# Optimization experiments

Measured on AMD Instinct MI355X. Metric: run time of the kernel, lower is better.

Reference implementation:

```python
import jax, jax.numpy as jnp
import numpy as np

K = 10  # module init kwarg k; Kmin selects k+1 then drops the self-distance column


def setup_inputs() -> dict:
    key = jax.random.key(0)
    N, D = 16384, 512
    obs = jax.random.normal(key, (N, D), dtype=jnp.float32)
    return {"obs": obs}


def reference(obs):
    # sa_ent=False -> x = y = obs
    x = obs
    # (same math as ((x_i - y_j)**2).sum(), expressed as a dense GEMM)
    sq = jnp.sum(x * x, axis=-1)  # [N]
    d2 = sq[:, None] + sq[None, :] - 2.0 * (x @ x.T)  # [N, N]
    # k+1 smallest per row (self-distance 0 included), ascending order
    neg_vals, _ = jax.lax.top_k(-d2, K + 1)  # [N, K+1]
    smallest = -neg_vals
    # drop self column, clamp tiny negatives from the expansion, sqrt
    r = jnp.sqrt(jnp.maximum(smallest[:, 1:], 0.0))  # [N, K]
    # style == 'log_mean'
    return jnp.log1p(jnp.mean(r, axis=-1))  # [N]
```

## Files before the change

### kernel.cpp

```cpp
#include <hip/hip_runtime.h>
#include <math.h>

#define NPTS 16384
#define DIM  512
#define KSEL 11
#define NSPLIT 8
#define CPS   (NPTS / NSPLIT)
#define BMM   256
#define BMT   128
#define BN    64
#define MITERS (CPS / BN)
#define TITERS 16
#define TCH   4096
#define STRIPB 8192
#define CAP   24
#define QS    22.0f

typedef __attribute__((ext_vector_type(4))) int i32x4;

__device__ __forceinline__ void gload_lds16(const void* g, void* l) {
    __builtin_amdgcn_global_load_lds(
        (const __attribute__((address_space(1))) void*)g,
        (__attribute__((address_space(3))) void*)l, 16, 0, 0);
}

__device__ __forceinline__ void pinreg(i32x4& v) { asm volatile("" : "+v"(v)); }
__device__ __forceinline__ void pini(int& v)     { asm volatile("" : "+v"(v)); }

__device__ __forceinline__ int topk_scan_i(const int* v, int n, int* a) {
    #pragma unroll
    for (int p = 0; p < KSEL; ++p) a[p] = v[p];
    int mx = a[0];
    #pragma unroll
    for (int p = 1; p < KSEL; ++p) mx = max(mx, a[p]);
    for (int i = KSEL; i < n; ++i) {
        const int x = v[i];
        if (x < mx) {
            bool done = false;
            #pragma unroll
            for (int p = 0; p < KSEL; ++p) {
                const bool rep = (!done) && (a[p] == mx);
                a[p] = rep ? x : a[p];
                done = done || rep;
            }
            mx = a[0];
            #pragma unroll
            for (int p = 1; p < KSEL; ++p) mx = max(mx, a[p]);
        }
    }
    return mx;
}

__global__ void prep_convert(const float* __restrict__ obs, char* __restrict__ obsb,
                             int* __restrict__ sqi) {
    const int wv = threadIdx.x >> 6, ln = threadIdx.x & 63;
    const int row = blockIdx.x * 4 + wv;
    const float4* s = (const float4*)(obs + (unsigned long)row * DIM + ln * 8);
    const float4 a = s[0], b = s[1];
    float xs[8] = {a.x, a.y, a.z, a.w, b.x, b.y, b.z, b.w};
    unsigned long u = 0ul;
    int ssum = 0;
    #pragma unroll
    for (int j = 0; j < 8; ++j) {
        const int q = __float2int_rn(fminf(fmaxf(xs[j] * QS, -127.f), 127.f));
        ssum += q * q;
        u |= ((unsigned long)((unsigned)q & 0xffu)) << (8 * j);
    }
    *(unsigned long*)(obsb + (unsigned long)(row >> 4) * STRIPB + (ln >> 3) * 1024
                      + ((ln >> 1) & 3) * 256 + (row & 15) * 16 + (ln & 1) * 8) = u;
    #pragma unroll
    for (int off = 32; off; off >>= 1) ssum += __shfl_xor(ssum, off);
    if (ln == 0) sqi[row] = ssum;
}

#define STAGE(BUF, CITER) do {                                                  \
        const char* gs_ = obsb + (unsigned long)((C0 >> 4) + 4 * (CITER)) * STRIPB \
                          + wv * 8192 + ln * 16;                                \
        char* lb_ = &Braw[BUF][0] + wv * 8192;                                  \
        _Pragma("unroll")                                                       \
        for (int r_ = 0; r_ < 8; ++r_)                                          \
            gload_lds16(gs_ + r_ * 1024, lb_ + r_ * 1024);                      \
    } while (0)

#define GEMM_BODY(CUR, CITER)                                                   \
        const char* bp = &Braw[CUR][0];                                         \
        i32x4 acc[2][4] = {{{0,0,0,0},{0,0,0,0},{0,0,0,0},{0,0,0,0}},           \
                           {{0,0,0,0},{0,0,0,0},{0,0,0,0},{0,0,0,0}}};          \
        _Pragma("unroll")                                                       \
        for (int cg = 0; cg < 4; ++cg) {                                        \
            _Pragma("unroll")                                                   \
            for (int t = 0; t < 8; ++t) {                                       \
                const i32x4 b = *(const i32x4*)(bp + cg * STRIPB + t * 1024 + lfrag); \
                acc[0][cg] = __builtin_amdgcn_mfma_i32_16x16x64_i8(b, afrag[0][t], acc[0][cg], 0, 0, 0); \
                acc[1][cg] = __builtin_amdgcn_mfma_i32_16x16x64_i8(b, afrag[1][t], acc[1][cg], 0, 0, 0); \
            }                                                                   \
        }                                                                       \
        i32x4 sqv[4];                                                           \
        _Pragma("unroll")                                                       \
        for (int cg_ = 0; cg_ < 4; ++cg_)                                       \
            sqv[cg_] = *(const i32x4*)(sqi + C0 + (CITER) * BN + cg_ * 16 + kc * 4);

#define DIST(S, CG, R) (sqr[S] + sqv[CG][R] - 2 * acc[S][CG][R])

#define LOAD_AFRAG() do {                                                       \
        _Pragma("unroll")                                                       \
        for (int s = 0; s < 2; ++s) {                                           \
            const unsigned long sbase = (unsigned long)((R0 >> 4) + wv * 2 + s) * STRIPB; \
            _Pragma("unroll")                                                   \
            for (int t = 0; t < 8; ++t) {                                       \
                afrag[s][t] = *(const i32x4*)(obsb + sbase + t * 1024 + lfrag); \
                pinreg(afrag[s][t]);                                            \
            }                                                                   \
            sqr[s] = sqi[wrow0 + s * 16 + lr];                                  \
            pini(sqr[s]);                                                       \
        }                                                                       \
    } while (0)

__global__ __launch_bounds__(256, 2) void thresh_pass(
    const char* __restrict__ obsb, const int* __restrict__ sqi,
    int* __restrict__ Tv)
{
    __shared__ __align__(16) char Braw[2][BN * 512];

    const int tid = threadIdx.x;
    const int wv = tid >> 6, ln = tid & 63;
    const int q  = blockIdx.x >> 7;
    const int rt = blockIdx.x & 127;
    const int R0 = rt * BMT;
    const int C0 = q * TCH;
    const int wrow0 = R0 + wv * 32;
    const int lr = ln & 15;
    const int kc = ln >> 4;
    const int lfrag = kc * 256 + lr * 16;

    i32x4 afrag[2][8];
    int sqr[2];
    LOAD_AFRAG();

    int segmin[2][16];
    #pragma unroll
    for (int s = 0; s < 2; ++s)
        #pragma unroll
        for (int p = 0; p < 16; ++p) segmin[s][p] = 0x7FFFFFFF;

    STAGE(0, 0);
    __syncthreads();
    #pragma unroll 2
    for (int it = 0; it < TITERS; ++it) {
        const int cur = it & 1;
        if (it + 1 < TITERS) STAGE(cur ^ 1, it + 1);
        GEMM_BODY(cur, it);
        #pragma unroll
        for (int s = 0; s < 2; ++s)
            #pragma unroll
            for (int cg = 0; cg < 4; ++cg)
                #pragma unroll
                for (int r = 0; r < 4; ++r)
                    segmin[s][cg * 4 + r] = min(segmin[s][cg * 4 + r], DIST(s, cg, r));
        __syncthreads();
    }

    int* mins = (int*)&Braw[0][0];
    #pragma unroll
    for (int s = 0; s < 2; ++s)
        #pragma unroll
        for (int p = 0; p < 16; ++p)
            mins[(wv * 32 + s * 16 + lr) * 65 + kc * 16 + p] = segmin[s][p];
    __syncthreads();
    if (tid < BMT) {
        int a[KSEL];
        topk_scan_i(mins + tid * 65, 64, a);
        #pragma unroll
        for (int p = 0; p < KSEL; ++p)
            Tv[(unsigned long)(R0 + tid) * (4 * KSEL) + q * KSEL + p] = a[p];
    }
}

__global__ void tmerge(const int* __restrict__ Tv, int* __restrict__ T) {
    const int row = blockIdx.x * 256 + threadIdx.x;
    int a[KSEL];
    T[row] = topk_scan_i(Tv + (unsigned long)row * (4 * KSEL), 4 * KSEL, a);
}

__global__ __launch_bounds__(256, 2) void knn_main(
    const char* __restrict__ obsb, const int* __restrict__ sqi,
    const int* __restrict__ T, int* __restrict__ cnt,
    int* __restrict__ vals)
{
    __shared__ __align__(16) char Braw[2][BN * 512];
    __shared__ unsigned lcnt[BMM];

    const int tid = threadIdx.x;
    const int wv = tid >> 6, ln = tid & 63;
    const int sp = blockIdx.x >> 6;
    const int rt = blockIdx.x & 63;
    const int R0 = rt * BMM;
    const int C0 = sp * CPS;
    const int wrow0 = R0 + wv * 64;
    const int lr = ln & 15;
    const int kc = ln >> 4;
    const int lfrag = kc * 256 + lr * 16;

    lcnt[tid] = 0u;

    i32x4 afrag[4][8];
    int sqr[4];
    #pragma unroll
    for (int s = 0; s < 4; ++s) {
        const unsigned long sbase = (unsigned long)((R0 >> 4) + wv * 4 + s) * STRIPB;
        #pragma unroll
        for (int t = 0; t < 8; ++t) {
            afrag[s][t] = *(const i32x4*)(obsb + sbase + t * 1024 + lfrag);
            pinreg(afrag[s][t]);
        }
        sqr[s] = sqi[wrow0 + s * 16 + lr];
        pini(sqr[s]);
    }

    unsigned lrow[4]; int tval[4]; int* vbase[4];
    #pragma unroll
    for (int s = 0; s < 4; ++s) {
        const int row = wrow0 + s * 16 + lr;
        lrow[s]  = wv * 64 + s * 16 + lr;
        tval[s]  = T[row];
        pini(tval[s]);
        vbase[s] = vals + ((unsigned long)row * NSPLIT + sp) * CAP;
    }

    STAGE(0, 0);
    __syncthreads();
    #pragma unroll 2
    for (int it = 0; it < MITERS; ++it) {
        const int cur = it & 1;
        if (it + 1 < MITERS) STAGE(cur ^ 1, it + 1);
        const char* bp = &Braw[cur][0];
        i32x4 acc[4][4];
        #pragma unroll
        for (int s_ = 0; s_ < 4; ++s_)
            #pragma unroll
            for (int c_ = 0; c_ < 4; ++c_) acc[s_][c_] = (i32x4){0, 0, 0, 0};
        #pragma unroll
        for (int cg = 0; cg < 4; ++cg) {
            #pragma unroll
            for (int t = 0; t < 8; ++t) {
                const i32x4 b = *(const i32x4*)(bp + cg * STRIPB + t * 1024 + lfrag);
                #pragma unroll
                for (int s_ = 0; s_ < 4; ++s_)
                    acc[s_][cg] = __builtin_amdgcn_mfma_i32_16x16x64_i8(
                        b, afrag[s_][t], acc[s_][cg], 0, 0, 0);
            }
        }
        i32x4 sqv[4];
        #pragma unroll
        for (int c_ = 0; c_ < 4; ++c_)
            sqv[c_] = *(const i32x4*)(sqi + C0 + it * BN + c_ * 16 + kc * 4);
        #pragma unroll
        for (int s_ = 0; s_ < 4; ++s_)
            #pragma unroll
            for (int cg = 0; cg < 4; ++cg)
                #pragma unroll
                for (int r = 0; r < 4; ++r) {
                    const int v_ = sqr[s_] + sqv[cg][r] - 2 * acc[s_][cg][r];
                    if (v_ <= tval[s_]) {
                        const unsigned i_ = atomicAdd(&lcnt[lrow[s_]], 1u);
                        if (i_ < CAP) vbase[s_][i_] = v_;
                    }
                }
        __syncthreads();
    }

    {
        const unsigned c = lcnt[tid];
        cnt[(unsigned long)(R0 + tid) * NSPLIT + sp] = (int)(c < CAP ? c : CAP);
    }
}

__global__ void merge_out(const int* __restrict__ cnt, const int* __restrict__ vals,
                          float* __restrict__ out) {
    const int row = blockIdx.x * 256 + threadIdx.x;
    int arr[KSEL];
    #pragma unroll
    for (int p = 0; p < KSEL; ++p) arr[p] = 0x7FFFFFFF;
    int mx = 0x7FFFFFFF;
    for (int q = 0; q < NSPLIT; ++q) {
        const int n = min(cnt[(unsigned long)row * NSPLIT + q], CAP);
        const int* base = vals + ((unsigned long)row * NSPLIT + q) * CAP;
        for (int i = 0; i < n; ++i) {
            const int x = base[i];
            if (x < mx) {
                bool done = false;
                #pragma unroll
                for (int p = 0; p < KSEL; ++p) {
                    const bool rep = (!done) && (arr[p] == mx);
                    arr[p] = rep ? x : arr[p];
                    done = done || rep;
                }
                mx = arr[0];
                #pragma unroll
                for (int p = 1; p < KSEL; ++p) mx = max(mx, arr[p]);
            }
        }
    }
    int mn = arr[0];
    #pragma unroll
    for (int p = 1; p < KSEL; ++p) mn = min(mn, arr[p]);
    float ssum = 0.f;
    #pragma unroll
    for (int p = 0; p < KSEL; ++p) ssum += sqrtf((float)max(arr[p], 0));
    const float smn = sqrtf((float)max(mn, 0));
    out[row] = log1pf((ssum - smn) * (0.1f / QS));
}

extern "C" void kernel_launch(void* const* d_in, const int* in_sizes, int n_in,
                              void* d_out, int out_size, void* d_ws, size_t ws_size,
                              hipStream_t stream) {
    const float* obs = (const float*)d_in[0];
    float* out = (float*)d_out;
    char* ws = (char*)d_ws;

    char* obsb = ws;
    int*  sqi  = (int*)(ws + (size_t)NPTS * 512);
    int*  T    = sqi + NPTS;
    int*  cnt  = T + NPTS;
    int*  vals = cnt + NPTS * NSPLIT;
    int*  Tv   = vals;

    prep_convert<<<NPTS / 4, 256, 0, stream>>>(obs, obsb, sqi);
    thresh_pass<<<128 * 4, 256, 0, stream>>>(obsb, sqi, Tv);
    tmerge<<<NPTS / 256, 256, 0, stream>>>(Tv, T);
    knn_main<<<64 * NSPLIT, 256, 0, stream>>>(obsb, sqi, T, cnt, vals);
    merge_out<<<NPTS / 256, 256, 0, stream>>>(cnt, vals, out);
}
```

Measured before the change: 267.4 us.

## Switch int8 distance GEMMs to 32x32x32 MFMA with 32-row strip layout

Replaces the 16x16x64 int8 MFMA tiles with 32x32x32 int8 MFMA in both the threshold pass and the main kNN pass. The packed int8 layout becomes 32-row strips so each lane loads its fragment with a single contiguous 16-byte read, and the column-index mapping for norms and the segment-min write-out is updated to match. Larger MFMA tiles issue fewer instructions and make fewer LDS B-fragment reads per output, but each accumulator is now 16 registers, which raises register pressure.

```diff
diff --git a/kernel.cpp b/kernel.cpp
--- a/kernel.cpp
+++ b/kernel.cpp
@@ -12,11 +12,12 @@
 #define MITERS (CPS / BN)
 #define TITERS 16
 #define TCH   4096
-#define STRIPB 8192
+#define STRIPB 16384
 #define CAP   24
 #define QS    22.0f
 
-typedef __attribute__((ext_vector_type(4))) int i32x4;
+typedef __attribute__((ext_vector_type(4)))  int i32x4;
+typedef __attribute__((ext_vector_type(16))) int i32x16;
 
 __device__ __forceinline__ void gload_lds16(const void* g, void* l) {
     __builtin_amdgcn_global_load_lds(
@@ -26,6 +27,13 @@
 
 __device__ __forceinline__ void pinreg(i32x4& v) { asm volatile("" : "+v"(v)); }
 __device__ __forceinline__ void pini(int& v)     { asm volatile("" : "+v"(v)); }
+
+__device__ __forceinline__ i32x16 zero16i() {
+    i32x16 z;
+    #pragma unroll
+    for (int i = 0; i < 16; ++i) z[i] = 0;
+    return z;
+}
 
 __device__ __forceinline__ int topk_scan_i(const int* v, int n, int* a) {
     #pragma unroll
@@ -66,15 +74,15 @@
         ssum += q * q;
         u |= ((unsigned long)((unsigned)q & 0xffu)) << (8 * j);
     }
-    *(unsigned long*)(obsb + (unsigned long)(row >> 4) * STRIPB + (ln >> 3) * 1024
-                      + ((ln >> 1) & 3) * 256 + (row & 15) * 16 + (ln & 1) * 8) = u;
+    *(unsigned long*)(obsb + (unsigned long)(row >> 5) * STRIPB + (ln >> 2) * 1024
+                      + ((ln >> 1) & 1) * 512 + (row & 31) * 16 + (ln & 1) * 8) = u;
     #pragma unroll
     for (int off = 32; off; off >>= 1) ssum += __shfl_xor(ssum, off);
     if (ln == 0) sqi[row] = ssum;
 }
 
 #define STAGE(BUF, CITER) do {                                                  \
-        const char* gs_ = obsb + (unsigned long)((C0 >> 4) + 4 * (CITER)) * STRIPB \
+        const char* gs_ = obsb + (unsigned long)((C0 >> 5) + 2 * (CITER)) * STRIPB \
                           + wv * 8192 + ln * 16;                                \
         char* lb_ = &Braw[BUF][0] + wv * 8192;                                  \
         _Pragma("unroll")                                                       \
@@ -82,39 +90,7 @@
             gload_lds16(gs_ + r_ * 1024, lb_ + r_ * 1024);                      \
     } while (0)
 
-#define GEMM_BODY(CUR, CITER)                                                   \
-        const char* bp = &Braw[CUR][0];                                         \
-        i32x4 acc[2][4] = {{{0,0,0,0},{0,0,0,0},{0,0,0,0},{0,0,0,0}},           \
-                           {{0,0,0,0},{0,0,0,0},{0,0,0,0},{0,0,0,0}}};          \
-        _Pragma("unroll")                                                       \
-        for (int cg = 0; cg < 4; ++cg) {                                        \
-            _Pragma("unroll")                                                   \
-            for (int t = 0; t < 8; ++t) {                                       \
-                const i32x4 b = *(const i32x4*)(bp + cg * STRIPB + t * 1024 + lfrag); \
-                acc[0][cg] = __builtin_amdgcn_mfma_i32_16x16x64_i8(b, afrag[0][t], acc[0][cg], 0, 0, 0); \
-                acc[1][cg] = __builtin_amdgcn_mfma_i32_16x16x64_i8(b, afrag[1][t], acc[1][cg], 0, 0, 0); \
-            }                                                                   \
-        }                                                                       \
-        i32x4 sqv[4];                                                           \
-        _Pragma("unroll")                                                       \
-        for (int cg_ = 0; cg_ < 4; ++cg_)                                       \
-            sqv[cg_] = *(const i32x4*)(sqi + C0 + (CITER) * BN + cg_ * 16 + kc * 4);
-
-#define DIST(S, CG, R) (sqr[S] + sqv[CG][R] - 2 * acc[S][CG][R])
-
-#define LOAD_AFRAG() do {                                                       \
-        _Pragma("unroll")                                                       \
-        for (int s = 0; s < 2; ++s) {                                           \
-            const unsigned long sbase = (unsigned long)((R0 >> 4) + wv * 2 + s) * STRIPB; \
-            _Pragma("unroll")                                                   \
-            for (int t = 0; t < 8; ++t) {                                       \
-                afrag[s][t] = *(const i32x4*)(obsb + sbase + t * 1024 + lfrag); \
-                pinreg(afrag[s][t]);                                            \
-            }                                                                   \
-            sqr[s] = sqi[wrow0 + s * 16 + lr];                                  \
-            pini(sqr[s]);                                                       \
-        }                                                                       \
-    } while (0)
+#define COLIDX(CG, RQ) ((CG) * 32 + (RQ) * 8 + (ln >> 5) * 4)
 
 __global__ __launch_bounds__(256, 2) void thresh_pass(
     const char* __restrict__ obsb, const int* __restrict__ sqi,
@@ -129,19 +105,25 @@
     const int R0 = rt * BMT;
     const int C0 = q * TCH;
     const int wrow0 = R0 + wv * 32;
-    const int lr = ln & 15;
-    const int kc = ln >> 4;
-    const int lfrag = kc * 256 + lr * 16;
-
-    i32x4 afrag[2][8];
-    int sqr[2];
-    LOAD_AFRAG();
+
+    i32x4 afrag[16];
+    int sqr;
+    {
+        const unsigned long sbase = (unsigned long)((R0 >> 5) + wv) * STRIPB;
+        #pragma unroll
+        for (int t = 0; t < 16; ++t) {
+            afrag[t] = *(const i32x4*)(obsb + sbase + t * 1024 + ln * 16);
+            pinreg(afrag[t]);
+        }
+        sqr = sqi[wrow0 + (ln & 31)];
+        pini(sqr);
+    }
 
     int segmin[2][16];
     #pragma unroll
-    for (int s = 0; s < 2; ++s)
-        #pragma unroll
-        for (int p = 0; p < 16; ++p) segmin[s][p] = 0x7FFFFFFF;
+    for (int cg = 0; cg < 2; ++cg)
+        #pragma unroll
+        for (int r = 0; r < 16; ++r) segmin[cg][r] = 0x7FFFFFFF;
 
     STAGE(0, 0);
     __syncthreads();
@@ -149,23 +131,37 @@
     for (int it = 0; it < TITERS; ++it) {
         const int cur = it & 1;
         if (it + 1 < TITERS) STAGE(cur ^ 1, it + 1);
-        GEMM_BODY(cur, it);
-        #pragma unroll
-        for (int s = 0; s < 2; ++s)
-            #pragma unroll
-            for (int cg = 0; cg < 4; ++cg)
-                #pragma unroll
-                for (int r = 0; r < 4; ++r)
-                    segmin[s][cg * 4 + r] = min(segmin[s][cg * 4 + r], DIST(s, cg, r));
+        const char* bp = &Braw[cur][0];
+        i32x16 acc[2] = {zero16i(), zero16i()};
+        #pragma unroll
+        for (int cg = 0; cg < 2; ++cg)
+            #pragma unroll
+            for (int t = 0; t < 16; ++t) {
+                const i32x4 b = *(const i32x4*)(bp + cg * STRIPB + t * 1024 + ln * 16);
+                acc[cg] = __builtin_amdgcn_mfma_i32_32x32x32_i8(b, afrag[t], acc[cg], 0, 0, 0);
+            }
+        i32x4 sqv[2][4];
+        #pragma unroll
+        for (int cg = 0; cg < 2; ++cg)
+            #pragma unroll
+            for (int rq = 0; rq < 4; ++rq)
+                sqv[cg][rq] = *(const i32x4*)(sqi + C0 + it * BN + COLIDX(cg, rq));
+        #pragma unroll
+        for (int cg = 0; cg < 2; ++cg)
+            #pragma unroll
+            for (int r = 0; r < 16; ++r) {
+                const int v = sqr + sqv[cg][r >> 2][r & 3] - 2 * acc[cg][r];
+                segmin[cg][r] = min(segmin[cg][r], v);
+            }
         __syncthreads();
     }
 
     int* mins = (int*)&Braw[0][0];
     #pragma unroll
-    for (int s = 0; s < 2; ++s)
-        #pragma unroll
-        for (int p = 0; p < 16; ++p)
-            mins[(wv * 32 + s * 16 + lr) * 65 + kc * 16 + p] = segmin[s][p];
+    for (int cg = 0; cg < 2; ++cg)
+        #pragma unroll
+        for (int r = 0; r < 16; ++r)
+            mins[(wv * 32 + (ln & 31)) * 65 + (ln >> 5) * 32 + cg * 16 + r] = segmin[cg][r];
     __syncthreads();
     if (tid < BMT) {
         int a[KSEL];
@@ -197,31 +193,28 @@
     const int R0 = rt * BMM;
     const int C0 = sp * CPS;
     const int wrow0 = R0 + wv * 64;
-    const int lr = ln & 15;
-    const int kc = ln >> 4;
-    const int lfrag = kc * 256 + lr * 16;
 
     lcnt[tid] = 0u;
 
-    i32x4 afrag[4][8];
-    int sqr[4];
-    #pragma unroll
-    for (int s = 0; s < 4; ++s) {
-        const unsigned long sbase = (unsigned long)((R0 >> 4) + wv * 4 + s) * STRIPB;
-        #pragma unroll
-        for (int t = 0; t < 8; ++t) {
-            afrag[s][t] = *(const i32x4*)(obsb + sbase + t * 1024 + lfrag);
+    i32x4 afrag[2][16];
+    int sqr[2];
+    #pragma unroll
+    for (int s = 0; s < 2; ++s) {
+        const unsigned long sbase = (unsigned long)((R0 >> 5) + wv * 2 + s) * STRIPB;
+        #pragma unroll
+        for (int t = 0; t < 16; ++t) {
+            afrag[s][t] = *(const i32x4*)(obsb + sbase + t * 1024 + ln * 16);
             pinreg(afrag[s][t]);
         }
-        sqr[s] = sqi[wrow0 + s * 16 + lr];
+        sqr[s] = sqi[wrow0 + s * 32 + (ln & 31)];
         pini(sqr[s]);
     }
 
-    unsigned lrow[4]; int tval[4]; int* vbase[4];
-    #pragma unroll
-    for (int s = 0; s < 4; ++s) {
-        const int row = wrow0 + s * 16 + lr;
-        lrow[s]  = wv * 64 + s * 16 + lr;
+    unsigned lrow[2]; int tval[2]; int* vbase[2];
+    #pragma unroll
+    for (int s = 0; s < 2; ++s) {
+        const int row = wrow0 + s * 32 + (ln & 31);
+        lrow[s]  = wv * 64 + s * 32 + (ln & 31);
         tval[s]  = T[row];
         pini(tval[s]);
         vbase[s] = vals + ((unsigned long)row * NSPLIT + sp) * CAP;
@@ -234,36 +227,31 @@
         const int cur = it & 1;
         if (it + 1 < MITERS) STAGE(cur ^ 1, it + 1);
         const char* bp = &Braw[cur][0];
-        i32x4 acc[4][4];
-        #pragma unroll
-        for (int s_ = 0; s_ < 4; ++s_)
-            #pragma unroll
-            for (int c_ = 0; c_ < 4; ++c_) acc[s_][c_] = (i32x4){0, 0, 0, 0};
-        #pragma unroll
-        for (int cg = 0; cg < 4; ++cg) {
-            #pragma unroll
-            for (int t = 0; t < 8; ++t) {
-                const i32x4 b = *(const i32x4*)(bp + cg * STRIPB + t * 1024 + lfrag);
+        i32x16 acc[2][2] = {{zero16i(), zero16i()}, {zero16i(), zero16i()}};
+        #pragma unroll
+        for (int cg = 0; cg < 2; ++cg)
+            #pragma unroll
+            for (int t = 0; t < 16; ++t) {
+                const i32x4 b = *(const i32x4*)(bp + cg * STRIPB + t * 1024 + ln * 16);
+                acc[0][cg] = __builtin_amdgcn_mfma_i32_32x32x32_i8(b, afrag[0][t], acc[0][cg], 0, 0, 0);
+                acc[1][cg] = __builtin_amdgcn_mfma_i32_32x32x32_i8(b, afrag[1][t], acc[1][cg], 0, 0, 0);
+            }
+        i32x4 sqv[2][4];
+        #pragma unroll
+        for (int cg = 0; cg < 2; ++cg)
+            #pragma unroll
+            for (int rq = 0; rq < 4; ++rq)
+                sqv[cg][rq] = *(const i32x4*)(sqi + C0 + it * BN + COLIDX(cg, rq));
+        #pragma unroll
+        for (int s = 0; s < 2; ++s)
+            #pragma unroll
+            for (int cg = 0; cg < 2; ++cg)
                 #pragma unroll
-                for (int s_ = 0; s_ < 4; ++s_)
-                    acc[s_][cg] = __builtin_amdgcn_mfma_i32_16x16x64_i8(
-                        b, afrag[s_][t], acc[s_][cg], 0, 0, 0);
-            }
-        }
-        i32x4 sqv[4];
-        #pragma unroll
-        for (int c_ = 0; c_ < 4; ++c_)
-            sqv[c_] = *(const i32x4*)(sqi + C0 + it * BN + c_ * 16 + kc * 4);
-        #pragma unroll
-        for (int s_ = 0; s_ < 4; ++s_)
-            #pragma unroll
-            for (int cg = 0; cg < 4; ++cg)
-                #pragma unroll
-                for (int r = 0; r < 4; ++r) {
-                    const int v_ = sqr[s_] + sqv[cg][r] - 2 * acc[s_][cg][r];
-                    if (v_ <= tval[s_]) {
-                        const unsigned i_ = atomicAdd(&lcnt[lrow[s_]], 1u);
-                        if (i_ < CAP) vbase[s_][i_] = v_;
+                for (int r = 0; r < 16; ++r) {
+                    const int v_ = sqr[s] + sqv[cg][r >> 2][r & 3] - 2 * acc[s][cg][r];
+                    if (v_ <= tval[s]) {
+                        const unsigned i_ = atomicAdd(&lcnt[lrow[s]], 1u);
+                        if (i_ < CAP) vbase[s][i_] = v_;
                     }
                 }
         __syncthreads();
```

Measured after the change: 283.3 us. 1.06x slower.
